# Optimization experiments

Measured on AMD Instinct MI355X. Metric: run time of the kernel, lower is better.

Reference implementation:

```python
import jax, jax.numpy as jnp
import numpy as np

B, L, D, H = 4, 1024, 1024, 16
E = 16384
HD = D // H  # head dim = 64


def setup_inputs() -> dict:
    key = jax.random.key(0)
    k1, k2, k3, k4 = jax.random.split(key, 4)
    x = jax.random.normal(k1, (B, L, D), dtype=jnp.float32)
    edges = jax.random.randint(k2, (E, 2), 0, L, dtype=jnp.int32)
    w_qkv = jax.random.normal(k3, (3 * D, D), dtype=jnp.float32) * 0.02
    b_qkv = jnp.zeros((3 * D,), dtype=jnp.float32)
    w_out = jax.random.normal(k4, (D, D), dtype=jnp.float32) * 0.02
    b_out = jnp.zeros((D,), dtype=jnp.float32)
    return {"x": x, "edges": edges, "w_qkv": w_qkv, "b_qkv": b_qkv,
            "w_out": w_out, "b_out": b_out}


def reference(x, edges, w_qkv, b_qkv, w_out, b_out):
    # Build symmetric boolean adjacency mask [L, L]; True = edge present.
    adj = jnp.zeros((L, L), dtype=bool)
    adj = adj.at[edges[:, 0], edges[:, 1]].set(True)
    adj = adj.at[edges[:, 1], edges[:, 0]].set(True)

    # Fused QKV projection (torch MultiheadAttention in_proj).
    qkv = x @ w_qkv.T + b_qkv                      # [B, L, 3D]
    q, k, v = jnp.split(qkv, 3, axis=-1)           # each [B, L, D]

    def heads(t):  # [B, L, D] -> [B, H, L, HD]
        return t.reshape(B, L, H, HD).transpose(0, 2, 1, 3)

    q, k, v = heads(q), heads(k), heads(v)
    scale = 1.0 / np.sqrt(HD)
    scores = jnp.einsum('bhqd,bhkd->bhqk', q * scale, k)  # [B, H, L, L]
    # torch bool attn_mask: True means NOT allowed to attend -> -inf.
    scores = jnp.where(adj[None, None, :, :], -jnp.inf, scores)
    attn = jax.nn.softmax(scores, axis=-1)
    out = jnp.einsum('bhqk,bhkd->bhqd', attn, v)   # [B, H, L, HD]
    out = out.transpose(0, 2, 1, 3).reshape(B, L, D)
    return out @ w_out.T + b_out
```

## Files before the change

kernel.cpp:

```cpp
#include <hip/hip_runtime.h>
#include <hip/hip_bf16.h>
#include <stdint.h>

#define B_   4
#define L_   1024
#define D_   1024
#define H_   16
#define HD_  64
#define E_   16384
#define BH_  (B_*H_)
#define BL_  (B_*L_)

typedef __bf16 bf16;
typedef __bf16 bf16x8 __attribute__((ext_vector_type(8)));
typedef float  f32x4  __attribute__((ext_vector_type(4)));
typedef unsigned short u16x8 __attribute__((ext_vector_type(8)));

#if __has_builtin(__builtin_amdgcn_exp2f)
#define EXP2F(x) __builtin_amdgcn_exp2f(x)
#else
#define EXP2F(x) exp2f(x)
#endif

#define QSCALE 0.18033688011112042f

__device__ __forceinline__ void gload_lds16(const bf16* gsrc, bf16* lds_dst) {
  __builtin_amdgcn_global_load_lds(
      (const __attribute__((address_space(1))) unsigned int*)gsrc,
      (__attribute__((address_space(3))) unsigned int*)lds_dst,
      16, 0, 0);
}

__global__ __launch_bounds__(256) void k_castall(
    const void* __restrict__ x, const void* __restrict__ wq,
    const void* __restrict__ wo, const void* __restrict__ bq,
    const void* __restrict__ bo,
    const int* __restrict__ edges, unsigned long long* __restrict__ adj,
    bf16* __restrict__ xb, bf16* __restrict__ wqb, bf16* __restrict__ wob,
    float* __restrict__ bqf, float* __restrict__ bof,
    unsigned int* __restrict__ flag_out) {
  const int t = threadIdx.x;

  bool lf = false;
  {
    u16x8 u = *(const u16x8*)((const unsigned short*)wq + (size_t)t * 8);
#pragma unroll
    for (int q = 0; q < 8; ++q) lf |= (((u[q] >> 7) & 0xFF) >= 200);
  }
  const bool f = __any(lf);
  if (blockIdx.x == 0 && t == 0 && f) *flag_out = 1u;

  if (blockIdx.x < 64) {
    int i = blockIdx.x * 256 + t;
    int a = edges[2 * i], b = edges[2 * i + 1];
    atomicOr(&adj[a * 16 + (b >> 6)], 1ull << (b & 63));
    atomicOr(&adj[b * 16 + (a >> 6)], 1ull << (a & 63));
  }

  const long e = ((long)blockIdx.x * 256 + t) * 8;
  const long N0 = 4l << 20, N1 = N0 + (3l << 20), N2 = N1 + (1l << 20);
  const void* src;
  bf16* d16 = nullptr; float* d32 = nullptr; long j;
  if (e < N0)      { src = x;  d16 = xb;  j = e; }
  else if (e < N1) { src = wq; d16 = wqb; j = e - N0; }
  else if (e < N2) { src = wo; d16 = wob; j = e - N1; }
  else {
    long b = e - N2;
    if (b < 3072)      { src = bq; d32 = bqf; j = b; }
    else if (b < 4096) { src = bo; d32 = bof; j = b - 3072; }
    else return;
  }
  if (d16) {
    bf16x8 v;
    if (f) {
      const float* s = (const float*)src + j;
#pragma unroll
      for (int q = 0; q < 8; ++q) v[q] = (bf16)s[q];
    } else {
      v = *(const bf16x8*)((const bf16*)src + j);
    }
    *(bf16x8*)(d16 + j) = v;
  } else {
    if (f) {
      const f32x4* s = (const f32x4*)((const float*)src + j);
      f32x4 a = s[0], b2 = s[1];
      *(f32x4*)(d32 + j) = a;
      *((f32x4*)(d32 + j) + 1) = b2;
    } else {
      const bf16* s = (const bf16*)src + j;
#pragma unroll
      for (int q = 0; q < 8; ++q) d32[j + q] = (float)s[q];
    }
  }
}

__global__ __launch_bounds__(512, 4) void k_gemm_qkv(
    const bf16* __restrict__ A, const bf16* __restrict__ W,
    const float* __restrict__ bias,
    bf16* __restrict__ qb, bf16* __restrict__ kb, bf16* __restrict__ vb) {
  constexpr int K = 1024;
  __shared__ __align__(16) bf16 As[2 * 128 * 32];
  __shared__ __align__(16) bf16 Bs[2 * 128 * 32];

  const int t = threadIdx.x;
  const int lane = t & 63, w = t >> 6;
  const int wm = w >> 1, wn = w & 1;
  const int quad = lane >> 4, l16 = lane & 15;
  const int m0 = blockIdx.y * 128, n0 = blockIdx.x * 128;

  const bf16* Abase = A + m0 * K;
  const bf16* Wbase = W + n0 * K;

  const int srow = t >> 2;
  const int scol = (((t & 3) << 4) ^ (((srow >> 1) & 3) << 4)) >> 1;
  const bf16* asrc = Abase + srow * K + scol;
  const bf16* wsrc = Wbase + srow * K + scol;

  const int fo = ((quad * 16) ^ (((l16 >> 1) & 3) << 4)) >> 1;

  f32x4 acc[2][4] = {};

#define STAGE_AB(it1) do {                                 \
    const int bo_ = ((it1) & 1) * 4096;                    \
    gload_lds16(asrc + (it1) * 32, &As[bo_ + w * 512]);    \
    gload_lds16(wsrc + (it1) * 32, &Bs[bo_ + w * 512]);    \
  } while (0)

  STAGE_AB(0);

#pragma unroll 1
  for (int it = 0; it < 32; ++it) {
    const int bo = (it & 1) * 4096;

    if (it < 31) STAGE_AB(it + 1);

    if (it < 31) asm volatile("s_waitcnt vmcnt(2)" ::: "memory");
    else         asm volatile("s_waitcnt vmcnt(0)" ::: "memory");
    __builtin_amdgcn_s_barrier();

    bf16x8 af[2], bfv[4];
#pragma unroll
    for (int i = 0; i < 2; ++i)
      af[i] = *(const bf16x8*)&As[bo + (wm * 32 + i * 16 + l16) * 32 + fo];
#pragma unroll
    for (int j = 0; j < 4; ++j)
      bfv[j] = *(const bf16x8*)&Bs[bo + (wn * 64 + j * 16 + l16) * 32 + fo];
#pragma unroll
    for (int mi = 0; mi < 2; ++mi)
#pragma unroll
      for (int ni = 0; ni < 4; ++ni)
        acc[mi][ni] = __builtin_amdgcn_mfma_f32_16x16x32_bf16(
            af[mi], bfv[ni], acc[mi][ni], 0, 0, 0);
    __builtin_amdgcn_s_barrier();
  }
#undef STAGE_AB

#pragma unroll
  for (int ni = 0; ni < 4; ++ni) {
    int col = n0 + wn * 64 + ni * 16 + l16;
    float bv = bias[col];
    int which = col >> 10;
    int hcol = col & 1023;
    int h = hcol >> 6, hd = hcol & 63;
#pragma unroll
    for (int mi = 0; mi < 2; ++mi)
#pragma unroll
      for (int r = 0; r < 4; ++r) {
        int row = m0 + wm * 32 + mi * 16 + quad * 4 + r;
        int bb = row >> 10, l = row & 1023;
        int bh = bb * H_ + h;
        float v = acc[mi][ni][r] + bv;
        if (which == 0)      qb[(bh * L_ + l) * HD_ + hd] = (bf16)(v * QSCALE);
        else if (which == 1) kb[(bh * L_ + l) * HD_ + hd] = (bf16)v;
        else                 vb[(bh * HD_ + hd) * L_ + l] = (bf16)v;
      }
  }
}

__global__ __launch_bounds__(256, 4) void k_gemm_out(
    const bf16* __restrict__ A, const bf16* __restrict__ W,
    const float* __restrict__ bias, void* __restrict__ outv,
    const unsigned int* __restrict__ flag) {
  constexpr int K = 1024;
  __shared__ __align__(16) bf16 As[2 * 2048];
  __shared__ __align__(16) bf16 Bs[2 * 2048];

  const int t = threadIdx.x;
  const int lane = t & 63, w = t >> 6;
  const int wm = w >> 1, wn = w & 1;
  const int quad = lane >> 4, l16 = lane & 15;
  const int m0 = blockIdx.y * 64, n0 = blockIdx.x * 64;

  const bf16* Abase = A + m0 * K;
  const bf16* Wbase = W + n0 * K;

  const int srow = t >> 2;
  const int scol = (((t & 3) << 4) ^ (((srow >> 1) & 3) << 4)) >> 1;
  const bf16* asrc = Abase + srow * K + scol;
  const bf16* wsrc = Wbase + srow * K + scol;

  const int fo = ((quad * 16) ^ (((l16 >> 1) & 3) << 4)) >> 1;

  f32x4 acc[2][2] = {};

#define STAGE_O(it1) do {                                  \
    const int bo_ = ((it1) & 1) * 2048;                    \
    gload_lds16(asrc + (it1) * 32, &As[bo_ + w * 512]);    \
    gload_lds16(wsrc + (it1) * 32, &Bs[bo_ + w * 512]);    \
  } while (0)

  STAGE_O(0);

#pragma unroll 1
  for (int it = 0; it < 32; ++it) {
    const int bo = (it & 1) * 2048;

    if (it < 31) STAGE_O(it + 1);

    if (it < 31) asm volatile("s_waitcnt vmcnt(2)" ::: "memory");
    else         asm volatile("s_waitcnt vmcnt(0)" ::: "memory");
    __builtin_amdgcn_s_barrier();

    bf16x8 af[2], bfv[2];
#pragma unroll
    for (int i = 0; i < 2; ++i) {
      af[i]  = *(const bf16x8*)&As[bo + (wm * 32 + i * 16 + l16) * 32 + fo];
      bfv[i] = *(const bf16x8*)&Bs[bo + (wn * 32 + i * 16 + l16) * 32 + fo];
    }
#pragma unroll
    for (int mi = 0; mi < 2; ++mi)
#pragma unroll
      for (int ni = 0; ni < 2; ++ni)
        acc[mi][ni] = __builtin_amdgcn_mfma_f32_16x16x32_bf16(
            af[mi], bfv[ni], acc[mi][ni], 0, 0, 0);
    __builtin_amdgcn_s_barrier();
  }
#undef STAGE_O

  const bool f32out = (*flag != 0);
#pragma unroll
  for (int ni = 0; ni < 2; ++ni) {
    int col = n0 + wn * 32 + ni * 16 + l16;
    float bv = bias[col];
#pragma unroll
    for (int mi = 0; mi < 2; ++mi)
#pragma unroll
      for (int r = 0; r < 4; ++r) {
        int row = m0 + wm * 32 + mi * 16 + quad * 4 + r;
        float v = acc[mi][ni][r] + bv;
        if (f32out) ((float*)outv)[row * 1024 + col] = v;
        else        ((bf16*)outv)[row * 1024 + col] = (bf16)v;
      }
  }
}

__global__ __launch_bounds__(256, 4) void k_attn(
    const bf16* __restrict__ qb, const bf16* __restrict__ kb,
    const bf16* __restrict__ vb, const unsigned long long* __restrict__ adj,
    bf16* __restrict__ aout) {
  __shared__ __align__(16) bf16 Ks[2 * 64 * 64];
  __shared__ __align__(16) bf16 Vt[2 * 64 * 64];
  __shared__ __align__(16) bf16 Ps[64 * 64];

  const int t = threadIdx.x, lane = t & 63, w = t >> 6;
  const int quad = lane >> 4, l16 = lane & 15;
  const int bh = blockIdx.y, qt = blockIdx.x;
  const int q0 = qt * 64 + w * 16;

  const bf16* qbase = qb + (size_t)bh * (L_ * HD_);
  const bf16* kbase = kb + (size_t)bh * (L_ * HD_);
  const bf16* vbase = vb + (size_t)bh * (HD_ * L_);

  bf16x8 aq[2];
#pragma unroll
  for (int c = 0; c < 2; ++c)
    aq[c] = *(const bf16x8*)&qbase[(q0 + l16) * HD_ + c * 32 + quad * 8];

  const int vr = lane >> 3;
  const int scol = ((lane & 7) ^ vr) * 8;
  const bf16* ksrc0 = kbase + (w * 16 + vr) * HD_ + scol;
  const bf16* ksrc1 = kbase + (w * 16 + 8 + vr) * HD_ + scol;
  const bf16* vsrc0 = vbase + (w * 16 + vr) * L_ + scol;
  const bf16* vsrc1 = vbase + (w * 16 + 8 + vr) * L_ + scol;

  const unsigned long long* adjrow = adj + (size_t)(q0 + quad * 4) * 16;

  float l_acc[4] = {0.f, 0.f, 0.f, 0.f};
  f32x4 o_acc[4] = {};

  const int psoff = (quad * 16) ^ ((l16 & 7) << 4);
  const int pswrow = (w * 16 + quad * 4) * 64;

#define STAGE_KV(i1) do {                                          \
    const int bo_ = ((i1) & 1) * 4096;                             \
    gload_lds16(ksrc0 + (i1) * 4096, &Ks[bo_ + (w * 16) * 64]);     \
    gload_lds16(ksrc1 + (i1) * 4096, &Ks[bo_ + (w * 16 + 8) * 64]); \
    gload_lds16(vsrc0 + (i1) * 64,   &Vt[bo_ + (w * 16) * 64]);     \
    gload_lds16(vsrc1 + (i1) * 64,   &Vt[bo_ + (w * 16 + 8) * 64]); \
  } while (0)

  STAGE_KV(0);

#pragma unroll 1
  for (int i = 0; i < 16; ++i) {
    const int bufo = (i & 1) * 4096;

    unsigned long long wmask[4];
#pragma unroll
    for (int r = 0; r < 4; ++r) wmask[r] = adjrow[r * 16 + i];

    if (i < 15) STAGE_KV(i + 1);

    if (i < 15) asm volatile("s_waitcnt vmcnt(8)" ::: "memory");
    else        asm volatile("s_waitcnt vmcnt(4)" ::: "memory");
    __builtin_amdgcn_s_barrier();

    f32x4 s[4];
#pragma unroll
    for (int nt = 0; nt < 4; ++nt) {
      f32x4 z = {};
#pragma unroll
      for (int c = 0; c < 2; ++c) {
        bf16x8 bk = *(const bf16x8*)&Ks[bufo + (nt * 16 + l16) * 64 +
            ((psoff ^ (c << 6)) >> 1)];
        z = __builtin_amdgcn_mfma_f32_16x16x32_bf16(aq[c], bk, z, 0, 0, 0);
      }
      s[nt] = z;
    }

#pragma unroll
    for (int r = 0; r < 4; ++r) {
      unsigned long long wr = wmask[r] >> l16;
      float pr = 0.f;
#pragma unroll
      for (int nt = 0; nt < 4; ++nt) {
        float sv = s[nt][r];
        if ((wr >> (nt * 16)) & 1ull) sv = -60000.f;
        float p = EXP2F(sv);
        int colb = (nt * 32 + l16 * 2) ^ (((quad * 4 + r) & 7) << 4);
        Ps[pswrow + r * 64 + (colb >> 1)] = (bf16)p;
        pr += p;
      }
      l_acc[r] += pr;
    }

#pragma unroll
    for (int c = 0; c < 2; ++c) {
      bf16x8 ap = *(const bf16x8*)
          &Ps[(w * 16 + l16) * 64 + ((psoff ^ (c << 6)) >> 1)];
#pragma unroll
      for (int nt = 0; nt < 4; ++nt) {
        bf16x8 bv = *(const bf16x8*)
            &Vt[bufo + (nt * 16 + l16) * 64 + ((psoff ^ (c << 6)) >> 1)];
        o_acc[nt] = __builtin_amdgcn_mfma_f32_16x16x32_bf16(ap, bv, o_acc[nt], 0, 0, 0);
      }
    }
    __builtin_amdgcn_s_barrier();
  }
#undef STAGE_KV

#pragma unroll
  for (int x = 1; x < 16; x <<= 1)
#pragma unroll
    for (int r = 0; r < 4; ++r)
      l_acc[r] += __shfl_xor(l_acc[r], x, 64);

  const int bb = bh >> 4, h = bh & 15;
#pragma unroll
  for (int r = 0; r < 4; ++r) {
    const float inv = l_acc[r] > 0.f ? 1.f / l_acc[r] : 0.f;
    const int qrow = q0 + quad * 4 + r;
    bf16* orow = aout + ((size_t)(bb * L_ + qrow)) * D_ + h * HD_;
#pragma unroll
    for (int nt = 0; nt < 4; ++nt)
      orow[nt * 16 + l16] = (bf16)(o_acc[nt][r] * inv);
  }
}

extern "C" void kernel_launch(void* const* d_in, const int* in_sizes, int n_in,
                              void* d_out, int out_size, void* d_ws, size_t ws_size,
                              hipStream_t stream) {
  const void* x_raw  = d_in[0];
  const int*  edges  = (const int*)d_in[1];
  const void* wq_raw = d_in[2];
  const void* bq_raw = d_in[3];
  const void* wo_raw = d_in[4];
  const void* bo_raw = d_in[5];

  char* ws = (char*)d_ws;
  unsigned int*        flag = (unsigned int*)ws;
  unsigned long long*  adj  = (unsigned long long*)(ws + 1024);
  size_t off = 1024 + 131072;
  bf16* xb    = (bf16*)(ws + off); off += (size_t)BL_ * D_ * 2;
  bf16* wqkvb = (bf16*)(ws + off); off += (size_t)3 * D_ * D_ * 2;
  bf16* woutb = (bf16*)(ws + off); off += (size_t)D_ * D_ * 2;
  float* bqf  = (float*)(ws + off); off += 3 * D_ * 4;
  float* bof  = (float*)(ws + off); off += D_ * 4;
  bf16* qb    = (bf16*)(ws + off); off += (size_t)BH_ * L_ * HD_ * 2;
  bf16* kb    = (bf16*)(ws + off); off += (size_t)BH_ * L_ * HD_ * 2;
  bf16* vb    = (bf16*)(ws + off); off += (size_t)BH_ * L_ * HD_ * 2;
  bf16* abuf  = (bf16*)(ws + off);

  hipMemsetAsync(ws, 0, 1024 + 131072, stream);

  k_castall<<<dim3(4098), dim3(256), 0, stream>>>(
      x_raw, wq_raw, wo_raw, bq_raw, bo_raw, edges, adj,
      xb, wqkvb, woutb, bqf, bof, flag);

  k_gemm_qkv<<<dim3(24, 32), dim3(512), 0, stream>>>(
      xb, wqkvb, bqf, qb, kb, vb);
  k_attn<<<dim3(16, 64), dim3(256), 0, stream>>>(qb, kb, vb, adj, abuf);
  k_gemm_out<<<dim3(16, 64), dim3(256), 0, stream>>>(
      abuf, woutb, bof, d_out, flag);
}
```

Baseline: 188.0 us.

## Fuse all stages into one persistent cooperative kernel with grid syncs

Replaces the memset plus four kernel launches with a single cooperative persistent kernel. It loops over work units for the cast/adjacency, QKV GEMM, attention and output GEMM stages, separating them with grid.sync. The QKV GEMM is re-tiled to 256 threads, each wave computing a 64x64 sub-tile with 4x4 MFMA accumulators. The aim is to remove launch gaps and the separate memset. The cost is grid-wide barriers and fixed occupancy, which may hurt load balance and latency hiding. A fallback to the old multi-kernel path remains if the cooperative launch fails.

```diff
diff --git a/kernel.cpp b/kernel.cpp
--- a/kernel.cpp
+++ b/kernel.cpp
@@ -1,6 +1,9 @@
 #include <hip/hip_runtime.h>
 #include <hip/hip_bf16.h>
+#include <hip/hip_cooperative_groups.h>
 #include <stdint.h>
+
+namespace cg = cooperative_groups;
 
 #define B_   4
 #define L_   1024
@@ -29,6 +32,347 @@
       (const __attribute__((address_space(1))) unsigned int*)gsrc,
       (__attribute__((address_space(3))) unsigned int*)lds_dst,
       16, 0, 0);
+}
+
+__global__ __launch_bounds__(256, 4) void k_fused(
+    const void* __restrict__ x, const int* __restrict__ edges,
+    const void* __restrict__ wq, const void* __restrict__ bq,
+    const void* __restrict__ wo, const void* __restrict__ bo,
+    unsigned long long* __restrict__ adj, unsigned int* __restrict__ flag,
+    bf16* __restrict__ xb, bf16* __restrict__ wqb, bf16* __restrict__ wob,
+    float* __restrict__ bqf, float* __restrict__ bof,
+    bf16* __restrict__ qb, bf16* __restrict__ kb, bf16* __restrict__ vb,
+    bf16* __restrict__ abuf, void* __restrict__ outv) {
+  __shared__ __align__(16) bf16 smem[20480];
+  cg::grid_group grid = cg::this_grid();
+
+  const int t = threadIdx.x;
+  const int bid = blockIdx.x;
+  const int nblk = gridDim.x;
+  const int lane = t & 63, w = t >> 6;
+  const int quad = lane >> 4, l16 = lane & 15;
+
+#pragma unroll 1
+  for (int u = bid; u < 64; u += nblk) adj[u * 256 + t] = 0ull;
+  if (bid == 0 && t == 0) *flag = 0u;
+  grid.sync();
+
+  {
+    bool lf = false;
+    {
+      u16x8 uv = *(const u16x8*)((const unsigned short*)wq + (size_t)t * 8);
+#pragma unroll
+      for (int q = 0; q < 8; ++q) lf |= (((uv[q] >> 7) & 0xFF) >= 200);
+    }
+    const bool f = __any(lf);
+    if (bid == 0 && t == 0 && f) *flag = 1u;
+
+#pragma unroll 1
+    for (int u = bid; u < 64; u += nblk) {
+      int i = u * 256 + t;
+      int a = edges[2 * i], b = edges[2 * i + 1];
+      atomicOr(&adj[a * 16 + (b >> 6)], 1ull << (b & 63));
+      atomicOr(&adj[b * 16 + (a >> 6)], 1ull << (a & 63));
+    }
+
+    const long N0 = 4l << 20, N1 = N0 + (3l << 20), N2 = N1 + (1l << 20);
+#pragma unroll 1
+    for (int u = bid; u < 4098; u += nblk) {
+      const long e = ((long)u * 256 + t) * 8;
+      const void* src = nullptr;
+      bf16* d16 = nullptr; float* d32 = nullptr; long j = 0;
+      if (e < N0)      { src = x;  d16 = xb;  j = e; }
+      else if (e < N1) { src = wq; d16 = wqb; j = e - N0; }
+      else if (e < N2) { src = wo; d16 = wob; j = e - N1; }
+      else {
+        long b = e - N2;
+        if (b < 3072)      { src = bq; d32 = bqf; j = b; }
+        else if (b < 4096) { src = bo; d32 = bof; j = b - 3072; }
+      }
+      if (d16) {
+        bf16x8 v;
+        if (f) {
+          const float* s = (const float*)src + j;
+#pragma unroll
+          for (int q = 0; q < 8; ++q) v[q] = (bf16)s[q];
+        } else {
+          v = *(const bf16x8*)((const bf16*)src + j);
+        }
+        *(bf16x8*)(d16 + j) = v;
+      } else if (d32) {
+        if (f) {
+          const f32x4* s = (const f32x4*)((const float*)src + j);
+          f32x4 a2 = s[0], b2 = s[1];
+          *(f32x4*)(d32 + j) = a2;
+          *((f32x4*)(d32 + j) + 1) = b2;
+        } else {
+          const bf16* s = (const bf16*)src + j;
+#pragma unroll
+          for (int q = 0; q < 8; ++q) d32[j + q] = (float)s[q];
+        }
+      }
+    }
+  }
+  grid.sync();
+
+  {
+    bf16* As = smem;
+    bf16* Bs = smem + 8192;
+    const int wm = w >> 1, wn = w & 1;
+    const int srow = t >> 2;
+    const int scol = (((t & 3) << 4) ^ (((srow >> 1) & 3) << 4)) >> 1;
+    const int fo = ((quad * 16) ^ (((l16 >> 1) & 3) << 4)) >> 1;
+
+#pragma unroll 1
+    for (int u = bid; u < 768; u += nblk) {
+      const int bx = u % 24, by = u / 24;
+      const int m0 = by * 128, n0 = bx * 128;
+      const bf16* Abase = xb + m0 * 1024;
+      const bf16* Wbase = wqb + n0 * 1024;
+      const bf16* asrc0 = Abase + srow * 1024 + scol;
+      const bf16* asrc1 = Abase + (srow + 64) * 1024 + scol;
+      const bf16* wsrc0 = Wbase + srow * 1024 + scol;
+      const bf16* wsrc1 = Wbase + (srow + 64) * 1024 + scol;
+
+      f32x4 acc[4][4] = {};
+#define STG_QKV(it1) do {                                          \
+        const int bo_ = ((it1) & 1) * 4096;                        \
+        gload_lds16(asrc0 + (it1) * 32, &As[bo_ + w * 512]);        \
+        gload_lds16(asrc1 + (it1) * 32, &As[bo_ + 2048 + w * 512]); \
+        gload_lds16(wsrc0 + (it1) * 32, &Bs[bo_ + w * 512]);        \
+        gload_lds16(wsrc1 + (it1) * 32, &Bs[bo_ + 2048 + w * 512]); \
+      } while (0)
+      STG_QKV(0);
+#pragma unroll 1
+      for (int it = 0; it < 32; ++it) {
+        const int bo = (it & 1) * 4096;
+        if (it < 31) STG_QKV(it + 1);
+        if (it < 31) asm volatile("s_waitcnt vmcnt(4)" ::: "memory");
+        else         asm volatile("s_waitcnt vmcnt(0)" ::: "memory");
+        __builtin_amdgcn_s_barrier();
+        bf16x8 af[4], bfv[4];
+#pragma unroll
+        for (int i = 0; i < 4; ++i) {
+          af[i]  = *(const bf16x8*)&As[bo + (wm * 64 + i * 16 + l16) * 32 + fo];
+          bfv[i] = *(const bf16x8*)&Bs[bo + (wn * 64 + i * 16 + l16) * 32 + fo];
+        }
+#pragma unroll
+        for (int mi = 0; mi < 4; ++mi)
+#pragma unroll
+          for (int ni = 0; ni < 4; ++ni)
+            acc[mi][ni] = __builtin_amdgcn_mfma_f32_16x16x32_bf16(
+                af[mi], bfv[ni], acc[mi][ni], 0, 0, 0);
+        __builtin_amdgcn_s_barrier();
+      }
+#undef STG_QKV
+#pragma unroll
+      for (int ni = 0; ni < 4; ++ni) {
+        int col = n0 + wn * 64 + ni * 16 + l16;
+        float bv = bqf[col];
+        int which = col >> 10;
+        int hcol = col & 1023;
+        int h = hcol >> 6, hd = hcol & 63;
+#pragma unroll
+        for (int mi = 0; mi < 4; ++mi)
+#pragma unroll
+          for (int r = 0; r < 4; ++r) {
+            int row = m0 + wm * 64 + mi * 16 + quad * 4 + r;
+            int bb = row >> 10, l = row & 1023;
+            int bh = bb * H_ + h;
+            float v = acc[mi][ni][r] + bv;
+            if (which == 0)      qb[(bh * L_ + l) * HD_ + hd] = (bf16)(v * QSCALE);
+            else if (which == 1) kb[(bh * L_ + l) * HD_ + hd] = (bf16)v;
+            else                 vb[(bh * HD_ + hd) * L_ + l] = (bf16)v;
+          }
+      }
+    }
+  }
+  grid.sync();
+
+  {
+    bf16* Ks = smem;
+    bf16* Vt = smem + 8192;
+    bf16* Ps = smem + 16384;
+
+#pragma unroll 1
+    for (int u = bid; u < 1024; u += nblk) {
+      const int qt = u & 15, bh = u >> 4;
+      const int q0 = qt * 64 + w * 16;
+
+      const bf16* qbase = qb + (size_t)bh * (L_ * HD_);
+      const bf16* kbase = kb + (size_t)bh * (L_ * HD_);
+      const bf16* vbase = vb + (size_t)bh * (HD_ * L_);
+
+      bf16x8 aq[2];
+#pragma unroll
+      for (int c = 0; c < 2; ++c)
+        aq[c] = *(const bf16x8*)&qbase[(q0 + l16) * HD_ + c * 32 + quad * 8];
+
+      const int vr = lane >> 3;
+      const int scol = ((lane & 7) ^ vr) * 8;
+      const bf16* ksrc0 = kbase + (w * 16 + vr) * HD_ + scol;
+      const bf16* ksrc1 = kbase + (w * 16 + 8 + vr) * HD_ + scol;
+      const bf16* vsrc0 = vbase + (w * 16 + vr) * L_ + scol;
+      const bf16* vsrc1 = vbase + (w * 16 + 8 + vr) * L_ + scol;
+
+      const unsigned long long* adjrow = adj + (size_t)(q0 + quad * 4) * 16;
+
+      float l_acc[4] = {0.f, 0.f, 0.f, 0.f};
+      f32x4 o_acc[4] = {};
+
+      const int psoff = (quad * 16) ^ ((l16 & 7) << 4);
+      const int pswrow = (w * 16 + quad * 4) * 64;
+
+#define STG_KV(i1) do {                                              \
+        const int bo_ = ((i1) & 1) * 4096;                           \
+        gload_lds16(ksrc0 + (i1) * 4096, &Ks[bo_ + (w * 16) * 64]);     \
+        gload_lds16(ksrc1 + (i1) * 4096, &Ks[bo_ + (w * 16 + 8) * 64]); \
+        gload_lds16(vsrc0 + (i1) * 64,   &Vt[bo_ + (w * 16) * 64]);     \
+        gload_lds16(vsrc1 + (i1) * 64,   &Vt[bo_ + (w * 16 + 8) * 64]); \
+      } while (0)
+
+      STG_KV(0);
+
+#pragma unroll 1
+      for (int i = 0; i < 16; ++i) {
+        const int bufo = (i & 1) * 4096;
+
+        unsigned long long wmask[4];
+#pragma unroll
+        for (int r = 0; r < 4; ++r) wmask[r] = adjrow[r * 16 + i];
+
+        if (i < 15) STG_KV(i + 1);
+
+        if (i < 15) asm volatile("s_waitcnt vmcnt(8)" ::: "memory");
+        else        asm volatile("s_waitcnt vmcnt(4)" ::: "memory");
+        __builtin_amdgcn_s_barrier();
+
+        f32x4 s[4];
+#pragma unroll
+        for (int nt = 0; nt < 4; ++nt) {
+          f32x4 z = {};
+#pragma unroll
+          for (int c = 0; c < 2; ++c) {
+            bf16x8 bk = *(const bf16x8*)&Ks[bufo + (nt * 16 + l16) * 64 +
+                ((psoff ^ (c << 6)) >> 1)];
+            z = __builtin_amdgcn_mfma_f32_16x16x32_bf16(aq[c], bk, z, 0, 0, 0);
+          }
+          s[nt] = z;
+        }
+
+#pragma unroll
+        for (int r = 0; r < 4; ++r) {
+          unsigned long long wr = wmask[r] >> l16;
+          float pr = 0.f;
+#pragma unroll
+          for (int nt = 0; nt < 4; ++nt) {
+            float sv = s[nt][r];
+            if ((wr >> (nt * 16)) & 1ull) sv = -60000.f;
+            float p = EXP2F(sv);
+            int colb = (nt * 32 + l16 * 2) ^ (((quad * 4 + r) & 7) << 4);
+            Ps[pswrow + r * 64 + (colb >> 1)] = (bf16)p;
+            pr += p;
+          }
+          l_acc[r] += pr;
+        }
+
+#pragma unroll
+        for (int c = 0; c < 2; ++c) {
+          bf16x8 ap = *(const bf16x8*)
+              &Ps[(w * 16 + l16) * 64 + ((psoff ^ (c << 6)) >> 1)];
+#pragma unroll
+          for (int nt = 0; nt < 4; ++nt) {
+            bf16x8 bv = *(const bf16x8*)
+                &Vt[bufo + (nt * 16 + l16) * 64 + ((psoff ^ (c << 6)) >> 1)];
+            o_acc[nt] = __builtin_amdgcn_mfma_f32_16x16x32_bf16(ap, bv, o_acc[nt], 0, 0, 0);
+          }
+        }
+        __builtin_amdgcn_s_barrier();
+      }
+#undef STG_KV
+
+#pragma unroll
+      for (int xr = 1; xr < 16; xr <<= 1)
+#pragma unroll
+        for (int r = 0; r < 4; ++r)
+          l_acc[r] += __shfl_xor(l_acc[r], xr, 64);
+
+      const int bb = bh >> 4, h = bh & 15;
+#pragma unroll
+      for (int r = 0; r < 4; ++r) {
+        const float inv = l_acc[r] > 0.f ? 1.f / l_acc[r] : 0.f;
+        const int qrow = q0 + quad * 4 + r;
+        bf16* orow = abuf + ((size_t)(bb * L_ + qrow)) * D_ + h * HD_;
+#pragma unroll
+        for (int nt = 0; nt < 4; ++nt)
+          orow[nt * 16 + l16] = (bf16)(o_acc[nt][r] * inv);
+      }
+    }
+  }
+  grid.sync();
+
+  {
+    bf16* As = smem;
+    bf16* Bs = smem + 4096;
+    const bool f32out = (*(volatile unsigned int*)flag != 0);
+    const int wm = w >> 1, wn = w & 1;
+    const int srow = t >> 2;
+    const int scol = (((t & 3) << 4) ^ (((srow >> 1) & 3) << 4)) >> 1;
+    const int fo = ((quad * 16) ^ (((l16 >> 1) & 3) << 4)) >> 1;
+
+#pragma unroll 1
+    for (int u = bid; u < 1024; u += nblk) {
+      const int bx = u & 15, by = u >> 4;
+      const int m0 = by * 64, n0 = bx * 64;
+      const bf16* asrc = abuf + (m0 + srow) * 1024 + scol;
+      const bf16* wsrc = wob + (n0 + srow) * 1024 + scol;
+
+      f32x4 acc[2][2] = {};
+#define STG_O(it1) do {                                      \
+        const int bo_ = ((it1) & 1) * 2048;                  \
+        gload_lds16(asrc + (it1) * 32, &As[bo_ + w * 512]);  \
+        gload_lds16(wsrc + (it1) * 32, &Bs[bo_ + w * 512]);  \
+      } while (0)
+      STG_O(0);
+#pragma unroll 1
+      for (int it = 0; it < 32; ++it) {
+        const int bo = (it & 1) * 2048;
+        if (it < 31) STG_O(it + 1);
+        if (it < 31) asm volatile("s_waitcnt vmcnt(2)" ::: "memory");
+        else         asm volatile("s_waitcnt vmcnt(0)" ::: "memory");
+        __builtin_amdgcn_s_barrier();
+        bf16x8 af[2], bfv[2];
+#pragma unroll
+        for (int i = 0; i < 2; ++i) {
+          af[i]  = *(const bf16x8*)&As[bo + (wm * 32 + i * 16 + l16) * 32 + fo];
+          bfv[i] = *(const bf16x8*)&Bs[bo + (wn * 32 + i * 16 + l16) * 32 + fo];
+        }
+#pragma unroll
+        for (int mi = 0; mi < 2; ++mi)
+#pragma unroll
+          for (int ni = 0; ni < 2; ++ni)
+            acc[mi][ni] = __builtin_amdgcn_mfma_f32_16x16x32_bf16(
+                af[mi], bfv[ni], acc[mi][ni], 0, 0, 0);
+        __builtin_amdgcn_s_barrier();
+      }
+#undef STG_O
+      const bool fo32 = f32out;
+#pragma unroll
+      for (int ni = 0; ni < 2; ++ni) {
+        int col = n0 + wn * 32 + ni * 16 + l16;
+        float bv = bof[col];
+#pragma unroll
+        for (int mi = 0; mi < 2; ++mi)
+#pragma unroll
+          for (int r = 0; r < 4; ++r) {
+            int row = m0 + wm * 32 + mi * 16 + quad * 4 + r;
+            float v = acc[mi][ni][r] + bv;
+            if (fo32) ((float*)outv)[row * 1024 + col] = v;
+            else      ((bf16*)outv)[row * 1024 + col] = (bf16)v;
+          }
+      }
+    }
+  }
 }
 
 __global__ __launch_bounds__(256) void k_castall(
@@ -40,7 +384,6 @@
     float* __restrict__ bqf, float* __restrict__ bof,
     unsigned int* __restrict__ flag_out) {
   const int t = threadIdx.x;
-
   bool lf = false;
   {
     u16x8 u = *(const u16x8*)((const unsigned short*)wq + (size_t)t * 8);
@@ -49,14 +392,12 @@
   }
   const bool f = __any(lf);
   if (blockIdx.x == 0 && t == 0 && f) *flag_out = 1u;
-
   if (blockIdx.x < 64) {
     int i = blockIdx.x * 256 + t;
     int a = edges[2 * i], b = edges[2 * i + 1];
     atomicOr(&adj[a * 16 + (b >> 6)], 1ull << (b & 63));
     atomicOr(&adj[b * 16 + (a >> 6)], 1ull << (a & 63));
   }
-
   const long e = ((long)blockIdx.x * 256 + t) * 8;
   const long N0 = 4l << 20, N1 = N0 + (3l << 20), N2 = N1 + (1l << 20);
   const void* src;
@@ -101,43 +442,32 @@
   constexpr int K = 1024;
   __shared__ __align__(16) bf16 As[2 * 128 * 32];
   __shared__ __align__(16) bf16 Bs[2 * 128 * 32];
-
   const int t = threadIdx.x;
   const int lane = t & 63, w = t >> 6;
   const int wm = w >> 1, wn = w & 1;
   const int quad = lane >> 4, l16 = lane & 15;
   const int m0 = blockIdx.y * 128, n0 = blockIdx.x * 128;
-
   const bf16* Abase = A + m0 * K;
   const bf16* Wbase = W + n0 * K;
-
   const int srow = t >> 2;
   const int scol = (((t & 3) << 4) ^ (((srow >> 1) & 3) << 4)) >> 1;
   const bf16* asrc = Abase + srow * K + scol;
   const bf16* wsrc = Wbase + srow * K + scol;
-
   const int fo = ((quad * 16) ^ (((l16 >> 1) & 3) << 4)) >> 1;
-
   f32x4 acc[2][4] = {};
-
 #define STAGE_AB(it1) do {                                 \
     const int bo_ = ((it1) & 1) * 4096;                    \
     gload_lds16(asrc + (it1) * 32, &As[bo_ + w * 512]);    \
     gload_lds16(wsrc + (it1) * 32, &Bs[bo_ + w * 512]);    \
   } while (0)
-
   STAGE_AB(0);
-
 #pragma unroll 1
   for (int it = 0; it < 32; ++it) {
     const int bo = (it & 1) * 4096;
-
     if (it < 31) STAGE_AB(it + 1);
-
     if (it < 31) asm volatile("s_waitcnt vmcnt(2)" ::: "memory");
     else         asm volatile("s_waitcnt vmcnt(0)" ::: "memory");
     __builtin_amdgcn_s_barrier();
-
     bf16x8 af[2], bfv[4];
 #pragma unroll
     for (int i = 0; i < 2; ++i)
@@ -154,7 +484,6 @@
     __builtin_amdgcn_s_barrier();
   }
 #undef STAGE_AB
-
 #pragma unroll
   for (int ni = 0; ni < 4; ++ni) {
     int col = n0 + wn * 64 + ni * 16 + l16;
@@ -184,43 +513,32 @@
   constexpr int K = 1024;
   __shared__ __align__(16) bf16 As[2 * 2048];
   __shared__ __align__(16) bf16 Bs[2 * 2048];
-
   const int t = threadIdx.x;
   const int lane = t & 63, w = t >> 6;
   const int wm = w >> 1, wn = w & 1;
   const int quad = lane >> 4, l16 = lane & 15;
   const int m0 = blockIdx.y * 64, n0 = blockIdx.x * 64;
-
   const bf16* Abase = A + m0 * K;
   const bf16* Wbase = W + n0 * K;
-
   const int srow = t >> 2;
   const int scol = (((t & 3) << 4) ^ (((srow >> 1) & 3) << 4)) >> 1;
   const bf16* asrc = Abase + srow * K + scol;
   const bf16* wsrc = Wbase + srow * K + scol;
-
   const int fo = ((quad * 16) ^ (((l16 >> 1) & 3) << 4)) >> 1;
-
   f32x4 acc[2][2] = {};
-
 #define STAGE_O(it1) do {                                  \
     const int bo_ = ((it1) & 1) * 2048;                    \
     gload_lds16(asrc + (it1) * 32, &As[bo_ + w * 512]);    \
     gload_lds16(wsrc + (it1) * 32, &Bs[bo_ + w * 512]);    \
   } while (0)
-
   STAGE_O(0);
-
 #pragma unroll 1
   for (int it = 0; it < 32; ++it) {
     const int bo = (it & 1) * 2048;
-
     if (it < 31) STAGE_O(it + 1);
-
     if (it < 31) asm volatile("s_waitcnt vmcnt(2)" ::: "memory");
     else         asm volatile("s_waitcnt vmcnt(0)" ::: "memory");
     __builtin_amdgcn_s_barrier();
-
     bf16x8 af[2], bfv[2];
 #pragma unroll
     for (int i = 0; i < 2; ++i) {
@@ -236,7 +554,6 @@
     __builtin_amdgcn_s_barrier();
   }
 #undef STAGE_O
-
   const bool f32out = (*flag != 0);
 #pragma unroll
   for (int ni = 0; ni < 2; ++ni) {
@@ -261,36 +578,28 @@
   __shared__ __align__(16) bf16 Ks[2 * 64 * 64];
   __shared__ __align__(16) bf16 Vt[2 * 64 * 64];
   __shared__ __align__(16) bf16 Ps[64 * 64];
-
   const int t = threadIdx.x, lane = t & 63, w = t >> 6;
   const int quad = lane >> 4, l16 = lane & 15;
   const int bh = blockIdx.y, qt = blockIdx.x;
   const int q0 = qt * 64 + w * 16;
-
   const bf16* qbase = qb + (size_t)bh * (L_ * HD_);
   const bf16* kbase = kb + (size_t)bh * (L_ * HD_);
   const bf16* vbase = vb + (size_t)bh * (HD_ * L_);
-
   bf16x8 aq[2];
 #pragma unroll
   for (int c = 0; c < 2; ++c)
     aq[c] = *(const bf16x8*)&qbase[(q0 + l16) * HD_ + c * 32 + quad * 8];
-
   const int vr = lane >> 3;
   const int scol = ((lane & 7) ^ vr) * 8;
   const bf16* ksrc0 = kbase + (w * 16 + vr) * HD_ + scol;
   const bf16* ksrc1 = kbase + (w * 16 + 8 + vr) * HD_ + scol;
   const bf16* vsrc0 = vbase + (w * 16 + vr) * L_ + scol;
   const bf16* vsrc1 = vbase + (w * 16 + 8 + vr) * L_ + scol;
-
   const unsigned long long* adjrow = adj + (size_t)(q0 + quad * 4) * 16;
-
   float l_acc[4] = {0.f, 0.f, 0.f, 0.f};
   f32x4 o_acc[4] = {};
-
   const int psoff = (quad * 16) ^ ((l16 & 7) << 4);
   const int pswrow = (w * 16 + quad * 4) * 64;
-
 #define STAGE_KV(i1) do {                                          \
     const int bo_ = ((i1) & 1) * 4096;                             \
     gload_lds16(ksrc0 + (i1) * 4096, &Ks[bo_ + (w * 16) * 64]);     \
@@ -298,23 +607,17 @@
     gload_lds16(vsrc0 + (i1) * 64,   &Vt[bo_ + (w * 16) * 64]);     \
     gload_lds16(vsrc1 + (i1) * 64,   &Vt[bo_ + (w * 16 + 8) * 64]); \
   } while (0)
-
   STAGE_KV(0);
-
 #pragma unroll 1
   for (int i = 0; i < 16; ++i) {
     const int bufo = (i & 1) * 4096;
-
     unsigned long long wmask[4];
 #pragma unroll
     for (int r = 0; r < 4; ++r) wmask[r] = adjrow[r * 16 + i];
-
     if (i < 15) STAGE_KV(i + 1);
-
     if (i < 15) asm volatile("s_waitcnt vmcnt(8)" ::: "memory");
     else        asm volatile("s_waitcnt vmcnt(4)" ::: "memory");
     __builtin_amdgcn_s_barrier();
-
     f32x4 s[4];
 #pragma unroll
     for (int nt = 0; nt < 4; ++nt) {
@@ -327,7 +630,6 @@
       }
       s[nt] = z;
     }
-
 #pragma unroll
     for (int r = 0; r < 4; ++r) {
       unsigned long long wr = wmask[r] >> l16;
@@ -343,7 +645,6 @@
       }
       l_acc[r] += pr;
     }
-
 #pragma unroll
     for (int c = 0; c < 2; ++c) {
       bf16x8 ap = *(const bf16x8*)
@@ -358,13 +659,11 @@
     __builtin_amdgcn_s_barrier();
   }
 #undef STAGE_KV
-
 #pragma unroll
   for (int x = 1; x < 16; x <<= 1)
 #pragma unroll
     for (int r = 0; r < 4; ++r)
       l_acc[r] += __shfl_xor(l_acc[r], x, 64);
-
   const int bb = bh >> 4, h = bh & 15;
 #pragma unroll
   for (int r = 0; r < 4; ++r) {
@@ -401,15 +700,32 @@
   bf16* vb    = (bf16*)(ws + off); off += (size_t)BH_ * L_ * HD_ * 2;
   bf16* abuf  = (bf16*)(ws + off);
 
-  hipMemsetAsync(ws, 0, 1024 + 131072, stream);
-
-  k_castall<<<dim3(4098), dim3(256), 0, stream>>>(
-      x_raw, wq_raw, wo_raw, bq_raw, bo_raw, edges, adj,
-      xb, wqkvb, woutb, bqf, bof, flag);
-
-  k_gemm_qkv<<<dim3(24, 32), dim3(512), 0, stream>>>(
-      xb, wqkvb, bqf, qb, kb, vb);
-  k_attn<<<dim3(16, 64), dim3(256), 0, stream>>>(qb, kb, vb, adj, abuf);
-  k_gemm_out<<<dim3(16, 64), dim3(256), 0, stream>>>(
-      abuf, woutb, bof, d_out, flag);
+  int perCU = 0;
+  if (hipOccupancyMaxActiveBlocksPerMultiprocessor(&perCU, k_fused, 256, 0)
+          != hipSuccess || perCU <= 0)
+    perCU = 4;
+  int nb = perCU * 256;
+  if (nb > 1024) nb = 1024;
+
+  void* args[] = {
+    (void*)&x_raw, (void*)&edges, (void*)&wq_raw, (void*)&bq_raw,
+    (void*)&wo_raw, (void*)&bo_raw, (void*)&adj, (void*)&flag,
+    (void*)&xb, (void*)&wqkvb, (void*)&woutb, (void*)&bqf, (void*)&bof,
+    (void*)&qb, (void*)&kb, (void*)&vb, (void*)&abuf, (void*)&d_out };
+
+  hipError_t ce = hipLaunchCooperativeKernel(
+      k_fused, dim3(nb), dim3(256), args, 0, stream);
+
+  if (ce != hipSuccess) {
+    (void)hipGetLastError();
+    hipMemsetAsync(ws, 0, 1024 + 131072, stream);
+    k_castall<<<dim3(4098), dim3(256), 0, stream>>>(
+        x_raw, wq_raw, wo_raw, bq_raw, bo_raw, edges, adj,
+        xb, wqkvb, woutb, bqf, bof, flag);
+    k_gemm_qkv<<<dim3(24, 32), dim3(512), 0, stream>>>(
+        xb, wqkvb, bqf, qb, kb, vb);
+    k_attn<<<dim3(16, 64), dim3(256), 0, stream>>>(qb, kb, vb, adj, abuf);
+    k_gemm_out<<<dim3(16, 64), dim3(256), 0, stream>>>(
+        abuf, woutb, bof, d_out, flag);
+  }
 }
```

Result: slower. 446.2 us (+137.3%).
